# Kernel optimization log

Measured on AMD Instinct MI355X. Metric: run time of the kernel, lower is better.

Reference implementation:

```python
import jax, jax.numpy as jnp
import numpy as np

B, SQ, SK, H, NH = 2, 2048, 2048, 1024, 16
HD = H // NH  # 64


def setup_inputs() -> dict:
    key = jax.random.key(0)
    ks = jax.random.split(key, 12)
    s = 1.0 / np.sqrt(H)
    inp = {
        "query": jax.random.normal(ks[0], (B, SQ, H), jnp.float32),
        "key": jax.random.normal(ks[1], (B, SK, H), jnp.float32),
        "value": jax.random.normal(ks[2], (B, SK, H), jnp.float32),
        # lower-triangular causal mask [B, SQ, SK]; nonzero = attend
        "causal_mask": jnp.broadcast_to(
            jnp.tril(jnp.ones((SQ, SK), jnp.int32)), (B, SQ, SK)
        ),
        "Wq": jax.random.uniform(ks[3], (H, H), jnp.float32, -s, s),
        "bq": jnp.zeros((H,), jnp.float32),
        "Wk": jax.random.uniform(ks[4], (H, H), jnp.float32, -s, s),
        "bk": jnp.zeros((H,), jnp.float32),
        "Wv": jax.random.uniform(ks[5], (H, H), jnp.float32, -s, s),
        "bv": jnp.zeros((H,), jnp.float32),
        "Wo": jax.random.uniform(ks[6], (H, H), jnp.float32, -s, s),
        "bo": jnp.zeros((H,), jnp.float32),
        "ln_g": jnp.ones((H,), jnp.float32),
        "ln_b": jnp.zeros((H,), jnp.float32),
    }
    return inp


def _layer_norm(x, g, b, eps=1e-5):
    mu = jnp.mean(x, axis=-1, keepdims=True)
    var = jnp.var(x, axis=-1, keepdims=True)
    return (x - mu) * jax.lax.rsqrt(var + eps) * g + b


def reference(query, key, value, causal_mask, Wq, bq, Wk, bk, Wv, bv, Wo, bo, ln_g, ln_b):
    # projections (torch Linear: x @ W.T + b)
    q = (query @ Wq.T + bq).reshape(B, SQ, NH, HD)
    k = (key @ Wk.T + bk).reshape(B, SK, NH, HD)
    v = (value @ Wv.T + bv).reshape(B, SK, NH, HD)
    # scores [B, NH, SQ, SK]
    scores = jnp.einsum("bqhd,bkhd->bhqk", q, k) / np.sqrt(HD).astype(np.float32)
    scores = jnp.where(causal_mask[:, None, :, :] == 0, -jnp.inf, scores)
    attn = jax.nn.softmax(scores, axis=-1)
    # dropout is identity in eval mode
    out = jnp.einsum("bhqk,bkhd->bqhd", attn, v).reshape(B, SQ, H)
    out = out @ Wo.T + bo
    return _layer_norm(query + out, ln_g, ln_b)
```

## Files before the change

### kernel.cpp

```cpp
#include <hip/hip_runtime.h>
#include <hip/hip_bf16.h>

#define SQL 2048
#define SKL 2048
#define HH  1024
#define NHH 16
#define HDD 64
#define BB  2
#define MM  (BB*SQL)

typedef __attribute__((ext_vector_type(8))) short short8;
typedef __attribute__((ext_vector_type(4))) float f32x4;
typedef unsigned short u16;

__device__ inline u16 f2bf(float f) {
    unsigned int u = __float_as_uint(f);
    u += 0x7fffu + ((u >> 16) & 1u);
    return (u16)(u >> 16);
}

__device__ inline void gl_lds16(const void* g, void* l) {
    __builtin_amdgcn_global_load_lds(
        (const __attribute__((address_space(1))) unsigned int*)g,
        (__attribute__((address_space(3))) unsigned int*)l, 16, 0, 0);
}

__global__ __launch_bounds__(256) void cvt_bf16_kernel(const float* __restrict__ src,
                                                       u16* __restrict__ dst, int n) {
    int i = (blockIdx.x * 256 + threadIdx.x) * 4;
    if (i >= n) return;
    float4 v = *(const float4*)(src + i);
    ushort4 o;
    o.x = f2bf(v.x); o.y = f2bf(v.y); o.z = f2bf(v.z); o.w = f2bf(v.w);
    *(ushort4*)(dst + i) = o;
}

template<int MODE>
__global__ __launch_bounds__(256) void gemm_kernel(
    const u16* __restrict__ A0, const u16* __restrict__ A1, const u16* __restrict__ A2,
    const u16* __restrict__ W0, const u16* __restrict__ W1, const u16* __restrict__ W2,
    const float* __restrict__ b0, const float* __restrict__ b1, const float* __restrict__ b2,
    u16* __restrict__ o0, u16* __restrict__ o1, u16* __restrict__ o2,
    const float* __restrict__ resid, float* __restrict__ outf)
{
    const int z = blockIdx.z;
    const u16* A = (z == 0) ? A0 : (z == 1) ? A1 : A2;
    const u16* W = (z == 0) ? W0 : (z == 1) ? W1 : W2;
    const float* bias = (z == 0) ? b0 : (z == 1) ? b1 : b2;
    u16* outb = (z == 0) ? o0 : (z == 1) ? o1 : o2;
    const float scale = (MODE == 0 && z == 0) ? 0.125f : 1.0f;

    __shared__ u16 lds_a[128 * 32];
    __shared__ u16 lds_b[128 * 32];

    const int t = threadIdx.x;
    const int lane = t & 63;
    const int wv = t >> 6;
    const int wm = (wv >> 1) * 64, wn = (wv & 1) * 64;
    const int m0 = blockIdx.x * 128;
    const int n0 = blockIdx.y * 128;

    f32x4 acc[4][4];
#pragma unroll
    for (int i = 0; i < 4; i++)
#pragma unroll
        for (int j = 0; j < 4; j++) acc[i][j] = (f32x4){0.f, 0.f, 0.f, 0.f};

    const int arow = t >> 2, acol = (t & 3) * 8;

    for (int k0 = 0; k0 < HH; k0 += 32) {
        gl_lds16(A + (size_t)(m0 + arow) * HH + k0 + acol,       &lds_a[t * 8]);
        gl_lds16(A + (size_t)(m0 + 64 + arow) * HH + k0 + acol,  &lds_a[2048 + t * 8]);
        gl_lds16(W + (size_t)(n0 + arow) * HH + k0 + acol,       &lds_b[t * 8]);
        gl_lds16(W + (size_t)(n0 + 64 + arow) * HH + k0 + acol,  &lds_b[2048 + t * 8]);
        __syncthreads();
        short8 af[4], bf[4];
#pragma unroll
        for (int i = 0; i < 4; i++) {
            af[i] = *(const short8*)&lds_a[(wm + i * 16 + (lane & 15)) * 32 + (lane >> 4) * 8];
            bf[i] = *(const short8*)&lds_b[(wn + i * 16 + (lane & 15)) * 32 + (lane >> 4) * 8];
        }
#pragma unroll
        for (int i = 0; i < 4; i++)
#pragma unroll
            for (int j = 0; j < 4; j++)
                acc[i][j] = __builtin_amdgcn_mfma_f32_16x16x32_bf16(af[i], bf[j], acc[i][j], 0, 0, 0);
        __syncthreads();
    }

#pragma unroll
    for (int i = 0; i < 4; i++) {
#pragma unroll
        for (int j = 0; j < 4; j++) {
#pragma unroll
            for (int r = 0; r < 4; r++) {
                int row = m0 + wm + i * 16 + ((lane >> 4) << 2) + r;
                int col = n0 + wn + j * 16 + (lane & 15);
                float val = acc[i][j][r] + bias[col];
                if (MODE == 0) {
                    val *= scale;
                    int bi = row >> 11, s = row & 2047;
                    int head = col >> 6, d = col & 63;
                    outb[(((size_t)bi * NHH + head) * SQL + s) * HDD + d] = f2bf(val);
                } else {
                    val += resid[(size_t)row * HH + col];
                    outf[(size_t)row * HH + col] = val;
                }
            }
        }
    }
}

#define VP 72
#define PR 72

__global__ __launch_bounds__(256) void attn_kernel(
    const u16* __restrict__ qb, const u16* __restrict__ kb, const u16* __restrict__ vb,
    u16* __restrict__ attn_out)
{
    __shared__ u16 k_lds[64 * 64];
    __shared__ u16 v_t[64 * VP];
    __shared__ u16 p_lds[4 * 16 * PR];

    const int t = threadIdx.x;
    const int lane = t & 63;
    const int w = t >> 6;
    const int qt = (SQL / 64 - 1) - (blockIdx.x >> 5);
    const int bh = blockIdx.x & 31;
    const int q0 = qt * 64;

    const u16* qbase = qb + ((size_t)bh * SQL + q0 + w * 16 + (lane & 15)) * HDD + ((lane >> 4) * 8);
    short8 qf0 = *(const short8*)qbase;
    short8 qf1 = *(const short8*)(qbase + 32);

    float m_r[4], l_r[4];
    f32x4 o[4];
#pragma unroll
    for (int r = 0; r < 4; r++) { m_r[r] = -__builtin_inff(); l_r[r] = 0.f; }
#pragma unroll
    for (int j = 0; j < 4; j++) o[j] = (f32x4){0.f, 0.f, 0.f, 0.f};

    const int vkey = t & 63, vdg = t >> 6;
    u16* ppriv = &p_lds[w * 16 * PR];

    for (int kt = 0; kt <= qt; kt++) {
        const int k0 = kt * 64;
        {
            int i0 = t, i1 = 256 + t;
            gl_lds16(kb + ((size_t)bh * SKL + k0 + (i0 >> 3)) * HDD + (i0 & 7) * 8, &k_lds[i0 * 8]);
            gl_lds16(kb + ((size_t)bh * SKL + k0 + (i1 >> 3)) * HDD + (i1 & 7) * 8, &k_lds[i1 * 8]);
        }
        {
            const u16* vsrc = vb + ((size_t)bh * SKL + k0 + vkey) * HDD + vdg * 16;
            short8 v0 = *(const short8*)vsrc;
            short8 v1 = *(const short8*)(vsrc + 8);
#pragma unroll
            for (int j = 0; j < 8; j++) v_t[(vdg * 16 + j) * VP + vkey] = (u16)v0[j];
#pragma unroll
            for (int j = 0; j < 8; j++) v_t[(vdg * 16 + 8 + j) * VP + vkey] = (u16)v1[j];
        }
        __syncthreads();

        f32x4 s[4];
#pragma unroll
        for (int nt = 0; nt < 4; nt++) {
            s[nt] = (f32x4){0.f, 0.f, 0.f, 0.f};
            const u16* kr = &k_lds[(nt * 16 + (lane & 15)) * 64 + (lane >> 4) * 8];
            short8 kf0 = *(const short8*)kr;
            short8 kf1 = *(const short8*)(kr + 32);
            s[nt] = __builtin_amdgcn_mfma_f32_16x16x32_bf16(qf0, kf0, s[nt], 0, 0, 0);
            s[nt] = __builtin_amdgcn_mfma_f32_16x16x32_bf16(qf1, kf1, s[nt], 0, 0, 0);
        }
        if (kt == qt) {
            int qrow = q0 + w * 16 + ((lane >> 4) << 2);
            int colb = k0 + (lane & 15);
#pragma unroll
            for (int nt = 0; nt < 4; nt++)
#pragma unroll
                for (int r = 0; r < 4; r++)
                    if (colb + nt * 16 > qrow + r) s[nt][r] = -__builtin_inff();
        }
        float mx[4];
#pragma unroll
        for (int r = 0; r < 4; r++)
            mx[r] = fmaxf(fmaxf(s[0][r], s[1][r]), fmaxf(s[2][r], s[3][r]));
#pragma unroll
        for (int off = 8; off; off >>= 1)
#pragma unroll
            for (int r = 0; r < 4; r++) mx[r] = fmaxf(mx[r], __shfl_xor(mx[r], off, 16));
        float al[4];
#pragma unroll
        for (int r = 0; r < 4; r++) {
            float mn = fmaxf(m_r[r], mx[r]);
            al[r] = __expf(m_r[r] - mn);
            m_r[r] = mn;
        }
#pragma unroll
        for (int nt = 0; nt < 4; nt++)
#pragma unroll
            for (int r = 0; r < 4; r++) s[nt][r] = __expf(s[nt][r] - m_r[r]);
        float rs[4];
#pragma unroll
        for (int r = 0; r < 4; r++) rs[r] = s[0][r] + s[1][r] + s[2][r] + s[3][r];
#pragma unroll
        for (int off = 8; off; off >>= 1)
#pragma unroll
            for (int r = 0; r < 4; r++) rs[r] += __shfl_xor(rs[r], off, 16);
#pragma unroll
        for (int r = 0; r < 4; r++) l_r[r] = l_r[r] * al[r] + rs[r];
#pragma unroll
        for (int nt = 0; nt < 4; nt++)
#pragma unroll
            for (int r = 0; r < 4; r++) o[nt][r] *= al[r];

#pragma unroll
        for (int nt = 0; nt < 4; nt++)
#pragma unroll
            for (int r = 0; r < 4; r++)
                ppriv[(((lane >> 4) << 2) + r) * PR + nt * 16 + (lane & 15)] = f2bf(s[nt][r]);
        short8 pf0 = *(const short8*)&ppriv[(lane & 15) * PR + (lane >> 4) * 8];
        short8 pf1 = *(const short8*)&ppriv[(lane & 15) * PR + 32 + (lane >> 4) * 8];
#pragma unroll
        for (int nt = 0; nt < 4; nt++) {
            const u16* vr = &v_t[(nt * 16 + (lane & 15)) * VP + (lane >> 4) * 8];
            short8 vf0 = *(const short8*)vr;
            short8 vf1 = *(const short8*)(vr + 32);
            o[nt] = __builtin_amdgcn_mfma_f32_16x16x32_bf16(pf0, vf0, o[nt], 0, 0, 0);
            o[nt] = __builtin_amdgcn_mfma_f32_16x16x32_bf16(pf1, vf1, o[nt], 0, 0, 0);
        }
        __syncthreads();
    }

    float inv[4];
#pragma unroll
    for (int r = 0; r < 4; r++) inv[r] = 1.0f / l_r[r];
    const int b = bh >> 4, h = bh & 15;
#pragma unroll
    for (int nt = 0; nt < 4; nt++)
#pragma unroll
        for (int r = 0; r < 4; r++) {
            int srow = q0 + w * 16 + ((lane >> 4) << 2) + r;
            attn_out[((size_t)b * SQL + srow) * HH + h * HDD + nt * 16 + (lane & 15)] =
                f2bf(o[nt][r] * inv[r]);
        }
}

__global__ __launch_bounds__(256) void ln_kernel(const float* __restrict__ x,
                                                 const float* __restrict__ g,
                                                 const float* __restrict__ bb,
                                                 float* __restrict__ out)
{
    const int row = blockIdx.x;
    const int t = threadIdx.x;
    const float* xr = x + (size_t)row * HH;
    float4 v = *(const float4*)(xr + t * 4);
    float s1 = v.x + v.y + v.z + v.w;
    float s2 = v.x * v.x + v.y * v.y + v.z * v.z + v.w * v.w;
#pragma unroll
    for (int off = 32; off; off >>= 1) { s1 += __shfl_xor(s1, off); s2 += __shfl_xor(s2, off); }
    __shared__ float red[8];
    if ((t & 63) == 0) { red[(t >> 6) * 2] = s1; red[(t >> 6) * 2 + 1] = s2; }
    __syncthreads();
    s1 = red[0] + red[2] + red[4] + red[6];
    s2 = red[1] + red[3] + red[5] + red[7];
    float mu = s1 * (1.0f / HH);
    float var = s2 * (1.0f / HH) - mu * mu;
    float rstd = rsqrtf(var + 1e-5f);
    float4 gg = *(const float4*)(g + t * 4);
    float4 b4 = *(const float4*)(bb + t * 4);
    float4 o;
    o.x = (v.x - mu) * rstd * gg.x + b4.x;
    o.y = (v.y - mu) * rstd * gg.y + b4.y;
    o.z = (v.z - mu) * rstd * gg.z + b4.z;
    o.w = (v.w - mu) * rstd * gg.w + b4.w;
    *(float4*)(out + (size_t)row * HH + t * 4) = o;
}

extern "C" void kernel_launch(void* const* d_in, const int* in_sizes, int n_in,
                              void* d_out, int out_size, void* d_ws, size_t ws_size,
                              hipStream_t stream)
{
    const float* query = (const float*)d_in[0];
    const float* key   = (const float*)d_in[1];
    const float* value = (const float*)d_in[2];
    const float* Wq = (const float*)d_in[4];
    const float* bq = (const float*)d_in[5];
    const float* Wk = (const float*)d_in[6];
    const float* bk = (const float*)d_in[7];
    const float* Wv = (const float*)d_in[8];
    const float* bv = (const float*)d_in[9];
    const float* Wo = (const float*)d_in[10];
    const float* bo = (const float*)d_in[11];
    const float* ln_g = (const float*)d_in[12];
    const float* ln_b = (const float*)d_in[13];
    float* out = (float*)d_out;

    char* wp = (char*)d_ws;
    auto alloc = [&](size_t bytes) { void* p = (void*)wp; wp += (bytes + 255) & ~(size_t)255; return p; };
    const int nW = HH * HH;
    const int nX = MM * HH;
    u16* wqb = (u16*)alloc((size_t)nW * 2);
    u16* wkb = (u16*)alloc((size_t)nW * 2);
    u16* wvb = (u16*)alloc((size_t)nW * 2);
    u16* wob = (u16*)alloc((size_t)nW * 2);
    u16* xq  = (u16*)alloc((size_t)nX * 2);
    u16* xk  = (u16*)alloc((size_t)nX * 2);
    u16* xv  = (u16*)alloc((size_t)nX * 2);
    u16* qbuf = (u16*)alloc((size_t)nX * 2);
    u16* kbuf = (u16*)alloc((size_t)nX * 2);
    u16* vbuf = (u16*)alloc((size_t)nX * 2);
    u16* attnb = (u16*)alloc((size_t)nX * 2);
    float* projf = (float*)alloc((size_t)nX * 4);

    cvt_bf16_kernel<<<nX / 1024, 256, 0, stream>>>(query, xq, nX);
    cvt_bf16_kernel<<<nX / 1024, 256, 0, stream>>>(key,   xk, nX);
    cvt_bf16_kernel<<<nX / 1024, 256, 0, stream>>>(value, xv, nX);
    cvt_bf16_kernel<<<nW / 1024, 256, 0, stream>>>(Wq, wqb, nW);
    cvt_bf16_kernel<<<nW / 1024, 256, 0, stream>>>(Wk, wkb, nW);
    cvt_bf16_kernel<<<nW / 1024, 256, 0, stream>>>(Wv, wvb, nW);
    cvt_bf16_kernel<<<nW / 1024, 256, 0, stream>>>(Wo, wob, nW);

    gemm_kernel<0><<<dim3(32, 8, 3), 256, 0, stream>>>(
        xq, xk, xv, wqb, wkb, wvb, bq, bk, bv, qbuf, kbuf, vbuf, nullptr, nullptr);

    attn_kernel<<<1024, 256, 0, stream>>>(qbuf, kbuf, vbuf, attnb);

    gemm_kernel<1><<<dim3(32, 8, 1), 256, 0, stream>>>(
        attnb, attnb, attnb, wob, wob, wob, bo, bo, bo, nullptr, nullptr, nullptr, query, projf);

    ln_kernel<<<MM, 256, 0, stream>>>(projf, ln_g, ln_b, out);
}
```

Before: 295.6 us.

## Write V pre-transposed, swizzle LDS tiles, use exp2 softmax, fuse conversion kernels

The V projection GEMM now writes V in a transposed per-head layout, so the attention kernel can load V tiles straight into LDS with async copies instead of transposing element by element. LDS tiles in the GEMM and attention kernels use an XOR swizzle to avoid bank conflicts. Attention computes S transposed, so each lane holds one query row, and switches to exp2 with log2e folded into the Q scale. The seven fp32-to-bf16 conversion launches are merged into one. The V GEMM's transposed store scatters writes with a large stride, and the new lane mapping adds shuffles to rescale O.

```diff
diff --git a/kernel.cpp b/kernel.cpp
--- a/kernel.cpp
+++ b/kernel.cpp
@@ -10,6 +10,7 @@
 #define MM  (BB*SQL)
 
 typedef __attribute__((ext_vector_type(8))) short short8;
+typedef __attribute__((ext_vector_type(4))) short short4v;
 typedef __attribute__((ext_vector_type(4))) float f32x4;
 typedef unsigned short u16;
 
@@ -25,36 +26,51 @@
         (__attribute__((address_space(3))) unsigned int*)l, 16, 0, 0);
 }
 
-__global__ __launch_bounds__(256) void cvt_bf16_kernel(const float* __restrict__ src,
-                                                       u16* __restrict__ dst, int n) {
-    int i = (blockIdx.x * 256 + threadIdx.x) * 4;
-    if (i >= n) return;
-    float4 v = *(const float4*)(src + i);
-    ushort4 o;
-    o.x = f2bf(v.x); o.y = f2bf(v.y); o.z = f2bf(v.z); o.w = f2bf(v.w);
-    *(ushort4*)(dst + i) = o;
+__global__ __launch_bounds__(256) void cvt_all_kernel(
+    const float* __restrict__ q, const float* __restrict__ k, const float* __restrict__ v,
+    const float* __restrict__ wq, const float* __restrict__ wk,
+    const float* __restrict__ wv, const float* __restrict__ wo,
+    u16* __restrict__ xq, u16* __restrict__ xk, u16* __restrict__ xv,
+    u16* __restrict__ wqb, u16* __restrict__ wkb, u16* __restrict__ wvb, u16* __restrict__ wob)
+{
+    int b = blockIdx.x;
+    const float* src; u16* dst;
+    if      (b < 4096)  { src = q;  dst = xq; }
+    else if (b < 8192)  { src = k;  dst = xk;  b -= 4096; }
+    else if (b < 12288) { src = v;  dst = xv;  b -= 8192; }
+    else if (b < 13312) { src = wq; dst = wqb; b -= 12288; }
+    else if (b < 14336) { src = wk; dst = wkb; b -= 13312; }
+    else if (b < 15360) { src = wv; dst = wvb; b -= 14336; }
+    else                { src = wo; dst = wob; b -= 15360; }
+    int i = (b * 256 + threadIdx.x) * 4;
+    float4 vv = *(const float4*)(src + i);
+    ushort4 oo;
+    oo.x = f2bf(vv.x); oo.y = f2bf(vv.y); oo.z = f2bf(vv.z); oo.w = f2bf(vv.w);
+    *(ushort4*)(dst + i) = oo;
 }
 
 template<int MODE>
 __global__ __launch_bounds__(256) void gemm_kernel(
-    const u16* __restrict__ A0, const u16* __restrict__ A1, const u16* __restrict__ A2,
-    const u16* __restrict__ W0, const u16* __restrict__ W1, const u16* __restrict__ W2,
-    const float* __restrict__ b0, const float* __restrict__ b1, const float* __restrict__ b2,
-    u16* __restrict__ o0, u16* __restrict__ o1, u16* __restrict__ o2,
+    const u16* __restrict__ A0, const u16* __restrict__ A1,
+    const u16* __restrict__ W0, const u16* __restrict__ W1,
+    const float* __restrict__ bias0, const float* __restrict__ bias1,
+    u16* __restrict__ o0, u16* __restrict__ o1,
     const float* __restrict__ resid, float* __restrict__ outf)
 {
     const int z = blockIdx.z;
-    const u16* A = (z == 0) ? A0 : (z == 1) ? A1 : A2;
-    const u16* W = (z == 0) ? W0 : (z == 1) ? W1 : W2;
-    const float* bias = (z == 0) ? b0 : (z == 1) ? b1 : b2;
-    u16* outb = (z == 0) ? o0 : (z == 1) ? o1 : o2;
-    const float scale = (MODE == 0 && z == 0) ? 0.125f : 1.0f;
+    const u16* A = (MODE == 0 && z == 1) ? A1 : A0;
+    const u16* W = (MODE == 0 && z == 1) ? W1 : W0;
+    const float* bias = (MODE == 0 && z == 1) ? bias1 : bias0;
+    u16* outb = (MODE == 0 && z == 1) ? o1 : o0;
+    const float scale = (MODE == 0 && z == 0) ? 0.125f * 1.4426950408889634f : 1.0f;
 
     __shared__ u16 lds_a[128 * 32];
     __shared__ u16 lds_b[128 * 32];
 
     const int t = threadIdx.x;
     const int lane = t & 63;
+    const int quad = lane >> 4;
+    const int lo = lane & 15;
     const int wv = t >> 6;
     const int wm = (wv >> 1) * 64, wn = (wv & 1) * 64;
     const int m0 = blockIdx.x * 128;
@@ -66,25 +82,33 @@
 #pragma unroll
         for (int j = 0; j < 4; j++) acc[i][j] = (f32x4){0.f, 0.f, 0.f, 0.f};
 
-    const int arow = t >> 2, acol = (t & 3) * 8;
+    const int sl0 = t, sl1 = 256 + t;
+    const int r0 = sl0 >> 2, c0 = ((sl0 & 3) ^ ((r0 >> 1) & 3)) * 8;
+    const int r1 = sl1 >> 2, c1 = ((sl1 & 3) ^ ((r1 >> 1) & 3)) * 8;
 
     for (int k0 = 0; k0 < HH; k0 += 32) {
-        gl_lds16(A + (size_t)(m0 + arow) * HH + k0 + acol,       &lds_a[t * 8]);
-        gl_lds16(A + (size_t)(m0 + 64 + arow) * HH + k0 + acol,  &lds_a[2048 + t * 8]);
-        gl_lds16(W + (size_t)(n0 + arow) * HH + k0 + acol,       &lds_b[t * 8]);
-        gl_lds16(W + (size_t)(n0 + 64 + arow) * HH + k0 + acol,  &lds_b[2048 + t * 8]);
+        gl_lds16(A + (size_t)(m0 + r0) * HH + k0 + c0, &lds_a[sl0 * 8]);
+        gl_lds16(A + (size_t)(m0 + r1) * HH + k0 + c1, &lds_a[sl1 * 8]);
+        gl_lds16(W + (size_t)(n0 + r0) * HH + k0 + c0, &lds_b[sl0 * 8]);
+        gl_lds16(W + (size_t)(n0 + r1) * HH + k0 + c1, &lds_b[sl1 * 8]);
         __syncthreads();
         short8 af[4], bf[4];
 #pragma unroll
         for (int i = 0; i < 4; i++) {
-            af[i] = *(const short8*)&lds_a[(wm + i * 16 + (lane & 15)) * 32 + (lane >> 4) * 8];
-            bf[i] = *(const short8*)&lds_b[(wn + i * 16 + (lane & 15)) * 32 + (lane >> 4) * 8];
+            const int ra = wm + i * 16 + lo;
+            const int rb = wn + i * 16 + lo;
+            af[i] = *(const short8*)&lds_a[ra * 32 + ((quad ^ ((ra >> 1) & 3)) * 8)];
+            bf[i] = *(const short8*)&lds_b[rb * 32 + ((quad ^ ((rb >> 1) & 3)) * 8)];
         }
 #pragma unroll
         for (int i = 0; i < 4; i++)
 #pragma unroll
-            for (int j = 0; j < 4; j++)
-                acc[i][j] = __builtin_amdgcn_mfma_f32_16x16x32_bf16(af[i], bf[j], acc[i][j], 0, 0, 0);
+            for (int j = 0; j < 4; j++) {
+                if (MODE == 2)
+                    acc[i][j] = __builtin_amdgcn_mfma_f32_16x16x32_bf16(bf[j], af[i], acc[i][j], 0, 0, 0);
+                else
+                    acc[i][j] = __builtin_amdgcn_mfma_f32_16x16x32_bf16(af[i], bf[j], acc[i][j], 0, 0, 0);
+            }
         __syncthreads();
     }
 
@@ -94,153 +118,155 @@
         for (int j = 0; j < 4; j++) {
 #pragma unroll
             for (int r = 0; r < 4; r++) {
-                int row = m0 + wm + i * 16 + ((lane >> 4) << 2) + r;
-                int col = n0 + wn + j * 16 + (lane & 15);
-                float val = acc[i][j][r] + bias[col];
-                if (MODE == 0) {
-                    val *= scale;
-                    int bi = row >> 11, s = row & 2047;
-                    int head = col >> 6, d = col & 63;
-                    outb[(((size_t)bi * NHH + head) * SQL + s) * HDD + d] = f2bf(val);
+                if (MODE == 2) {
+                    int dg  = n0 + wn + j * 16 + quad * 4 + r;
+                    int tok = m0 + wm + i * 16 + lo;
+                    float val = acc[i][j][r] + bias[dg];
+                    int head = dg >> 6, d = dg & 63;
+                    int bi = tok >> 11, s = tok & 2047;
+                    outb[(((size_t)bi * NHH + head) * HDD + d) * SKL + s] = f2bf(val);
                 } else {
-                    val += resid[(size_t)row * HH + col];
-                    outf[(size_t)row * HH + col] = val;
+                    int row = m0 + wm + i * 16 + quad * 4 + r;
+                    int col = n0 + wn + j * 16 + lo;
+                    float val = acc[i][j][r] + bias[col];
+                    if (MODE == 0) {
+                        val *= scale;
+                        int bi = row >> 11, s = row & 2047;
+                        int head = col >> 6, d = col & 63;
+                        outb[(((size_t)bi * NHH + head) * SQL + s) * HDD + d] = f2bf(val);
+                    } else {
+                        val += resid[(size_t)row * HH + col];
+                        outf[(size_t)row * HH + col] = val;
+                    }
                 }
             }
         }
     }
 }
 
-#define VP 72
-#define PR 72
+#define PSTR 72
 
 __global__ __launch_bounds__(256) void attn_kernel(
-    const u16* __restrict__ qb, const u16* __restrict__ kb, const u16* __restrict__ vb,
+    const u16* __restrict__ qb, const u16* __restrict__ kb, const u16* __restrict__ vtb,
     u16* __restrict__ attn_out)
 {
     __shared__ u16 k_lds[64 * 64];
-    __shared__ u16 v_t[64 * VP];
-    __shared__ u16 p_lds[4 * 16 * PR];
+    __shared__ u16 vt_lds[64 * 64];
+    __shared__ u16 p_lds[4 * 16 * PSTR];
 
     const int t = threadIdx.x;
     const int lane = t & 63;
+    const int quad = lane >> 4;
+    const int lo = lane & 15;
     const int w = t >> 6;
     const int qt = (SQL / 64 - 1) - (blockIdx.x >> 5);
     const int bh = blockIdx.x & 31;
     const int q0 = qt * 64;
 
-    const u16* qbase = qb + ((size_t)bh * SQL + q0 + w * 16 + (lane & 15)) * HDD + ((lane >> 4) * 8);
+    const u16* qbase = qb + ((size_t)bh * SQL + q0 + w * 16 + lo) * HDD + quad * 8;
     short8 qf0 = *(const short8*)qbase;
     short8 qf1 = *(const short8*)(qbase + 32);
 
-    float m_r[4], l_r[4];
+    float m_s = -__builtin_inff(), l_s = 0.f;
     f32x4 o[4];
 #pragma unroll
-    for (int r = 0; r < 4; r++) { m_r[r] = -__builtin_inff(); l_r[r] = 0.f; }
-#pragma unroll
     for (int j = 0; j < 4; j++) o[j] = (f32x4){0.f, 0.f, 0.f, 0.f};
 
-    const int vkey = t & 63, vdg = t >> 6;
-    u16* ppriv = &p_lds[w * 16 * PR];
+    const int sl0 = t, sl1 = 256 + t;
+    const int r0 = sl0 >> 3, c0 = ((sl0 & 7) ^ (r0 & 7)) * 8;
+    const int r1 = sl1 >> 3, c1 = ((sl1 & 7) ^ (r1 & 7)) * 8;
+    const u16* kbh = kb + (size_t)bh * SKL * HDD;
+    const u16* vbh = vtb + (size_t)bh * HDD * SKL;
+    u16* ppriv = &p_lds[w * 16 * PSTR];
 
     for (int kt = 0; kt <= qt; kt++) {
         const int k0 = kt * 64;
-        {
-            int i0 = t, i1 = 256 + t;
-            gl_lds16(kb + ((size_t)bh * SKL + k0 + (i0 >> 3)) * HDD + (i0 & 7) * 8, &k_lds[i0 * 8]);
-            gl_lds16(kb + ((size_t)bh * SKL + k0 + (i1 >> 3)) * HDD + (i1 & 7) * 8, &k_lds[i1 * 8]);
-        }
-        {
-            const u16* vsrc = vb + ((size_t)bh * SKL + k0 + vkey) * HDD + vdg * 16;
-            short8 v0 = *(const short8*)vsrc;
-            short8 v1 = *(const short8*)(vsrc + 8);
-#pragma unroll
-            for (int j = 0; j < 8; j++) v_t[(vdg * 16 + j) * VP + vkey] = (u16)v0[j];
-#pragma unroll
-            for (int j = 0; j < 8; j++) v_t[(vdg * 16 + 8 + j) * VP + vkey] = (u16)v1[j];
-        }
+        gl_lds16(kbh + (size_t)(k0 + r0) * HDD + c0, &k_lds[sl0 * 8]);
+        gl_lds16(kbh + (size_t)(k0 + r1) * HDD + c1, &k_lds[sl1 * 8]);
+        gl_lds16(vbh + (size_t)r0 * SKL + k0 + c0, &vt_lds[sl0 * 8]);
+        gl_lds16(vbh + (size_t)r1 * SKL + k0 + c1, &vt_lds[sl1 * 8]);
         __syncthreads();
 
         f32x4 s[4];
 #pragma unroll
         for (int nt = 0; nt < 4; nt++) {
+            const int row = nt * 16 + lo;
+            short8 kf0 = *(const short8*)&k_lds[row * 64 + ((quad ^ (row & 7)) * 8)];
+            short8 kf1 = *(const short8*)&k_lds[row * 64 + (((4 + quad) ^ (row & 7)) * 8)];
             s[nt] = (f32x4){0.f, 0.f, 0.f, 0.f};
-            const u16* kr = &k_lds[(nt * 16 + (lane & 15)) * 64 + (lane >> 4) * 8];
-            short8 kf0 = *(const short8*)kr;
-            short8 kf1 = *(const short8*)(kr + 32);
-            s[nt] = __builtin_amdgcn_mfma_f32_16x16x32_bf16(qf0, kf0, s[nt], 0, 0, 0);
-            s[nt] = __builtin_amdgcn_mfma_f32_16x16x32_bf16(qf1, kf1, s[nt], 0, 0, 0);
+            s[nt] = __builtin_amdgcn_mfma_f32_16x16x32_bf16(kf0, qf0, s[nt], 0, 0, 0);
+            s[nt] = __builtin_amdgcn_mfma_f32_16x16x32_bf16(kf1, qf1, s[nt], 0, 0, 0);
         }
         if (kt == qt) {
-            int qrow = q0 + w * 16 + ((lane >> 4) << 2);
-            int colb = k0 + (lane & 15);
+            const int ql = w * 16 + lo;
 #pragma unroll
             for (int nt = 0; nt < 4; nt++)
 #pragma unroll
                 for (int r = 0; r < 4; r++)
-                    if (colb + nt * 16 > qrow + r) s[nt][r] = -__builtin_inff();
-        }
-        float mx[4];
-#pragma unroll
-        for (int r = 0; r < 4; r++)
-            mx[r] = fmaxf(fmaxf(s[0][r], s[1][r]), fmaxf(s[2][r], s[3][r]));
-#pragma unroll
-        for (int off = 8; off; off >>= 1)
-#pragma unroll
-            for (int r = 0; r < 4; r++) mx[r] = fmaxf(mx[r], __shfl_xor(mx[r], off, 16));
-        float al[4];
-#pragma unroll
-        for (int r = 0; r < 4; r++) {
-            float mn = fmaxf(m_r[r], mx[r]);
-            al[r] = __expf(m_r[r] - mn);
-            m_r[r] = mn;
-        }
+                    if (nt * 16 + quad * 4 + r > ql) s[nt][r] = -__builtin_inff();
+        }
+
+        float mx = s[0][0];
 #pragma unroll
         for (int nt = 0; nt < 4; nt++)
 #pragma unroll
-            for (int r = 0; r < 4; r++) s[nt][r] = __expf(s[nt][r] - m_r[r]);
-        float rs[4];
-#pragma unroll
-        for (int r = 0; r < 4; r++) rs[r] = s[0][r] + s[1][r] + s[2][r] + s[3][r];
-#pragma unroll
-        for (int off = 8; off; off >>= 1)
-#pragma unroll
-            for (int r = 0; r < 4; r++) rs[r] += __shfl_xor(rs[r], off, 16);
-#pragma unroll
-        for (int r = 0; r < 4; r++) l_r[r] = l_r[r] * al[r] + rs[r];
+            for (int r = 0; r < 4; r++) mx = fmaxf(mx, s[nt][r]);
+        mx = fmaxf(mx, __shfl_xor(mx, 16));
+        mx = fmaxf(mx, __shfl_xor(mx, 32));
+        float mnew = fmaxf(m_s, mx);
+        float al = __builtin_amdgcn_exp2f(m_s - mnew);
+        m_s = mnew;
+        float rs = 0.f;
 #pragma unroll
         for (int nt = 0; nt < 4; nt++)
 #pragma unroll
-            for (int r = 0; r < 4; r++) o[nt][r] *= al[r];
-
+            for (int r = 0; r < 4; r++) {
+                s[nt][r] = __builtin_amdgcn_exp2f(s[nt][r] - m_s);
+                rs += s[nt][r];
+            }
+        rs += __shfl_xor(rs, 16);
+        rs += __shfl_xor(rs, 32);
+        l_s = l_s * al + rs;
+
+        float alr[4];
+#pragma unroll
+        for (int r = 0; r < 4; r++) alr[r] = __shfl(al, quad * 4 + r, 16);
 #pragma unroll
         for (int nt = 0; nt < 4; nt++)
 #pragma unroll
-            for (int r = 0; r < 4; r++)
-                ppriv[(((lane >> 4) << 2) + r) * PR + nt * 16 + (lane & 15)] = f2bf(s[nt][r]);
-        short8 pf0 = *(const short8*)&ppriv[(lane & 15) * PR + (lane >> 4) * 8];
-        short8 pf1 = *(const short8*)&ppriv[(lane & 15) * PR + 32 + (lane >> 4) * 8];
+            for (int r = 0; r < 4; r++) o[nt][r] *= alr[r];
+
 #pragma unroll
         for (int nt = 0; nt < 4; nt++) {
-            const u16* vr = &v_t[(nt * 16 + (lane & 15)) * VP + (lane >> 4) * 8];
-            short8 vf0 = *(const short8*)vr;
-            short8 vf1 = *(const short8*)(vr + 32);
+            short4v pk;
+#pragma unroll
+            for (int r = 0; r < 4; r++) pk[r] = (short)f2bf(s[nt][r]);
+            *(short4v*)&ppriv[lo * PSTR + nt * 16 + quad * 4] = pk;
+        }
+        short8 pf0 = *(const short8*)&ppriv[lo * PSTR + quad * 8];
+        short8 pf1 = *(const short8*)&ppriv[lo * PSTR + 32 + quad * 8];
+
+#pragma unroll
+        for (int nt = 0; nt < 4; nt++) {
+            const int row = nt * 16 + lo;
+            short8 vf0 = *(const short8*)&vt_lds[row * 64 + ((quad ^ (row & 7)) * 8)];
+            short8 vf1 = *(const short8*)&vt_lds[row * 64 + (((4 + quad) ^ (row & 7)) * 8)];
             o[nt] = __builtin_amdgcn_mfma_f32_16x16x32_bf16(pf0, vf0, o[nt], 0, 0, 0);
             o[nt] = __builtin_amdgcn_mfma_f32_16x16x32_bf16(pf1, vf1, o[nt], 0, 0, 0);
         }
         __syncthreads();
     }
 
+    const int b = bh >> 4, h = bh & 15;
     float inv[4];
 #pragma unroll
-    for (int r = 0; r < 4; r++) inv[r] = 1.0f / l_r[r];
-    const int b = bh >> 4, h = bh & 15;
+    for (int r = 0; r < 4; r++) inv[r] = 1.0f / __shfl(l_s, quad * 4 + r, 16);
 #pragma unroll
     for (int nt = 0; nt < 4; nt++)
 #pragma unroll
         for (int r = 0; r < 4; r++) {
-            int srow = q0 + w * 16 + ((lane >> 4) << 2) + r;
-            attn_out[((size_t)b * SQL + srow) * HH + h * HDD + nt * 16 + (lane & 15)] =
+            int srow = q0 + w * 16 + quad * 4 + r;
+            attn_out[((size_t)b * SQL + srow) * HH + h * HDD + nt * 16 + lo] =
                 f2bf(o[nt][r] * inv[r]);
         }
 }
@@ -312,21 +338,18 @@
     u16* attnb = (u16*)alloc((size_t)nX * 2);
     float* projf = (float*)alloc((size_t)nX * 4);
 
-    cvt_bf16_kernel<<<nX / 1024, 256, 0, stream>>>(query, xq, nX);
-    cvt_bf16_kernel<<<nX / 1024, 256, 0, stream>>>(key,   xk, nX);
-    cvt_bf16_kernel<<<nX / 1024, 256, 0, stream>>>(value, xv, nX);
-    cvt_bf16_kernel<<<nW / 1024, 256, 0, stream>>>(Wq, wqb, nW);
-    cvt_bf16_kernel<<<nW / 1024, 256, 0, stream>>>(Wk, wkb, nW);
-    cvt_bf16_kernel<<<nW / 1024, 256, 0, stream>>>(Wv, wvb, nW);
-    cvt_bf16_kernel<<<nW / 1024, 256, 0, stream>>>(Wo, wob, nW);
-
-    gemm_kernel<0><<<dim3(32, 8, 3), 256, 0, stream>>>(
-        xq, xk, xv, wqb, wkb, wvb, bq, bk, bv, qbuf, kbuf, vbuf, nullptr, nullptr);
+    cvt_all_kernel<<<16384, 256, 0, stream>>>(query, key, value, Wq, Wk, Wv, Wo,
+                                              xq, xk, xv, wqb, wkb, wvb, wob);
+
+    gemm_kernel<0><<<dim3(32, 8, 2), 256, 0, stream>>>(
+        xq, xk, wqb, wkb, bq, bk, qbuf, kbuf, nullptr, nullptr);
+    gemm_kernel<2><<<dim3(32, 8, 1), 256, 0, stream>>>(
+        xv, xv, wvb, wvb, bv, bv, vbuf, vbuf, nullptr, nullptr);
 
     attn_kernel<<<1024, 256, 0, stream>>>(qbuf, kbuf, vbuf, attnb);
 
     gemm_kernel<1><<<dim3(32, 8, 1), 256, 0, stream>>>(
-        attnb, attnb, attnb, wob, wob, wob, bo, bo, bo, nullptr, nullptr, nullptr, query, projf);
+        attnb, attnb, wob, wob, bo, bo, nullptr, nullptr, query, projf);
 
     ln_kernel<<<MM, 256, 0, stream>>>(projf, ln_g, ln_b, out);
 }
```

Result: faster. 266.8 us (-9.7%).
